# Performance work log

Hardware: AMD Instinct MI355X
Metric: run time of the kernel (lower is better)

Reference implementation:

```python
import jax, jax.numpy as jnp
import numpy as np


def conv_block(x, w1, b1, w2, b2):
    # 1x1 convs == per-pixel channel matmuls. x: [b, C, H, W]
    h = jax.nn.relu(jnp.einsum('bchw,oc->bohw', x, w1) + b1[None, :, None, None])
    return jnp.einsum('bchw,oc->bohw', h, w2) + b2[None, :, None, None]


def setup_inputs() -> dict:
    key = jax.random.key(0)
    ks = jax.random.split(key, 9)
    C, Ck = 256, 256 // 8
    bs, H, W = 4, 64, 64
    s_in = 1.0 / np.sqrt(C)
    s_k = 1.0 / np.sqrt(Ck)
    F_input = jax.random.normal(ks[0], (bs, C, H, W), dtype=jnp.float32)
    return {
        'F_input': F_input,
        'w1a': jax.random.normal(ks[1], (Ck, C), dtype=jnp.float32) * s_in,
        'b1a': jax.random.normal(ks[2], (Ck,), dtype=jnp.float32) * s_in,
        'w1b': jax.random.normal(ks[3], (Ck, Ck), dtype=jnp.float32) * s_k,
        'b1b': jax.random.normal(ks[4], (Ck,), dtype=jnp.float32) * s_k,
        'w2a': jax.random.normal(ks[5], (Ck, C), dtype=jnp.float32) * s_in,
        'b2a': jax.random.normal(ks[6], (Ck,), dtype=jnp.float32) * s_in,
        'w2b': jax.random.normal(ks[7], (Ck, Ck), dtype=jnp.float32) * s_k,
        'b2b': jax.random.normal(ks[8], (Ck,), dtype=jnp.float32) * s_k,
    }


def reference(F_input, w1a, b1a, w1b, b1b, w2a, b2a, w2b, b2b):
    bs, C, H, W = F_input.shape
    N = H * W
    q = conv_block(F_input, w1a, b1a, w1b, b1b).reshape(bs, -1, N)  # [b, Ck, N]
    k = conv_block(F_input, w2a, b2a, w2b, b2b).reshape(bs, -1, N)  # [b, Ck, N]
    # mm_1[b, n, m] = sum_c q[b, c, n] * k[b, c, m]
    scores = jnp.einsum('bcn,bcm->bnm', q, k)  # [b, N, N]
    S = jax.nn.softmax(scores, axis=-1)
    Fr = F_input.reshape(bs, C, N)
    # bmm(F_reshape, S^T): out[b, c, n] = sum_m F[b, c, m] * S[b, n, m]
    mm2 = jnp.einsum('bcm,bnm->bcn', Fr, S).reshape(bs, C, H, W)
    return F_input + mm2
```

## Files before the change

### kernel.cpp

```cpp
#include <hip/hip_runtime.h>
#include <math.h>

typedef __attribute__((ext_vector_type(4))) float f32x4;
typedef __attribute__((ext_vector_type(8))) short bf16x8;
typedef __attribute__((ext_vector_type(2))) unsigned int uint2v;
typedef __attribute__((ext_vector_type(4))) unsigned int uint4v;

#define LOG2E 1.4426950408889634f
#define MT 32
#define NIT 128

static __device__ __forceinline__ unsigned short f2bf(float f) {
  union { float f; unsigned int i; } u; u.f = f;
  unsigned int r = u.i + 0x7fffu + ((u.i >> 16) & 1u);
  return (unsigned short)(r >> 16);
}

typedef __attribute__((address_space(3))) unsigned int lds_u32;
typedef __attribute__((address_space(1))) unsigned int g_u32;

static __device__ __forceinline__ void gload_lds16(const unsigned short* g,
                                                   const unsigned short* l) {
  __builtin_amdgcn_global_load_lds(
      (const g_u32*)(unsigned long long)g,
      (lds_u32*)(unsigned int)(unsigned long long)l, 16, 0, 0);
}

__global__ __launch_bounds__(256) void k_wprep(const float* __restrict__ w1a,
                                               const float* __restrict__ w2a,
                                               float* __restrict__ w1aT,
                                               float* __restrict__ w2aT) {
  int i = blockIdx.x * 256 + threadIdx.x;
  if (i < 32 * 256) {
    int o = i >> 8, c = i & 255;
    w1aT[c * 32 + o] = w1a[i];
    w2aT[c * 32 + o] = w2a[i];
  }
}

__global__ __launch_bounds__(256) void k_cvt(const float* __restrict__ F,
                                             unsigned short* __restrict__ Fbf) {
  size_t i = ((size_t)blockIdx.x * 256 + threadIdx.x) * 8;
  f32x4 a = *(const f32x4*)(F + i);
  f32x4 b = *(const f32x4*)(F + i + 4);
  unsigned int u0 = (unsigned int)f2bf(a[0]) | ((unsigned int)f2bf(a[1]) << 16);
  unsigned int u1 = (unsigned int)f2bf(a[2]) | ((unsigned int)f2bf(a[3]) << 16);
  unsigned int u2 = (unsigned int)f2bf(b[0]) | ((unsigned int)f2bf(b[1]) << 16);
  unsigned int u3 = (unsigned int)f2bf(b[2]) | ((unsigned int)f2bf(b[3]) << 16);
  uint4v v = {u0, u1, u2, u3};
  *(uint4v*)(Fbf + i) = v;
}

__global__ __launch_bounds__(128) void k_qk(
    const float* __restrict__ F,
    const float* __restrict__ w1aT, const float* __restrict__ b1a,
    const float* __restrict__ w1b,  const float* __restrict__ b1b,
    const float* __restrict__ w2aT, const float* __restrict__ b2a,
    const float* __restrict__ w2b,  const float* __restrict__ b2b,
    unsigned short* __restrict__ qT,
    unsigned short* __restrict__ kT) {
  const int p = blockIdx.x & 1;
  const int nflat = (blockIdx.x >> 1) * 128 + threadIdx.x;
  const int b = nflat >> 12, n = nflat & 4095;
  const float* wA = p ? w2aT : w1aT;
  const float* bA = p ? b2a : b1a;
  const float* wB = p ? w2b : w1b;
  const float* bB = p ? b2b : b1b;
  const float* Fp = F + ((size_t)b * 256) * 4096 + n;

  float h[32];
#pragma unroll
  for (int o = 0; o < 32; ++o) h[o] = 0.f;

  float fa[8], fb[8];
#pragma unroll
  for (int j = 0; j < 8; ++j) fa[j] = Fp[(size_t)j * 4096];

  for (int cc = 0; cc < 256; cc += 16) {
#pragma unroll
    for (int j = 0; j < 8; ++j) fb[j] = Fp[(size_t)(cc + 8 + j) * 4096];
#pragma unroll
    for (int j = 0; j < 8; ++j)
#pragma unroll
      for (int o = 0; o < 32; ++o) h[o] += wA[(cc + j) * 32 + o] * fa[j];
    if (cc + 16 < 256) {
#pragma unroll
      for (int j = 0; j < 8; ++j) fa[j] = Fp[(size_t)(cc + 16 + j) * 4096];
    }
#pragma unroll
    for (int j = 0; j < 8; ++j)
#pragma unroll
      for (int o = 0; o < 32; ++o) h[o] += wA[(cc + 8 + j) * 32 + o] * fb[j];
  }
#pragma unroll
  for (int o = 0; o < 32; ++o) h[o] = fmaxf(h[o] + bA[o], 0.f);

  unsigned int pack[16];
#pragma unroll
  for (int o2 = 0; o2 < 32; o2 += 2) {
    float s0 = bB[o2], s1 = bB[o2 + 1];
#pragma unroll
    for (int o = 0; o < 32; ++o) {
      s0 += wB[o2 * 32 + o] * h[o];
      s1 += wB[(o2 + 1) * 32 + o] * h[o];
    }
    if (p == 0) { s0 *= LOG2E; s1 *= LOG2E; }
    pack[o2 >> 1] = (unsigned int)f2bf(s0) | ((unsigned int)f2bf(s1) << 16);
  }
  unsigned short* dst = (p ? kT : qT) + (size_t)nflat * 32;
  uint4v* d4 = (uint4v*)dst;
#pragma unroll
  for (int i = 0; i < 4; ++i) {
    uint4v v = {pack[4 * i], pack[4 * i + 1], pack[4 * i + 2], pack[4 * i + 3]};
    d4[i] = v;
  }
}

__global__ __launch_bounds__(256, 1) void k_attn(
    const unsigned short* __restrict__ qT,
    const unsigned short* __restrict__ kT,
    const unsigned short* __restrict__ Fbf,
    const float* __restrict__ F,
    float* __restrict__ out) {
  __shared__ unsigned short Vt[3][256 * MT];
  __shared__ unsigned short Pb[2][64 * MT];
  __shared__ float scl[2][64];
  __shared__ float linv[64];

  const int tid = threadIdx.x;
  const int w = tid >> 6;
  const int lane = tid & 63;
  const int lo = lane & 15;
  const int hi = lane >> 4;

  const int bid = (int)blockIdx.x;
  const int swz = (bid & 7) * 32 + (bid >> 3);
  const int b = swz >> 6;
  const int n0 = (swz & 63) << 6;

  const bf16x8 qfrag = *(const bf16x8*)(
      qT + ((size_t)(b << 12) + n0 + (w << 4) + lo) * 32 + (hi << 3));
  const unsigned short* kTb = kT + ((size_t)(b << 12)) * 32;
  const unsigned short* Fb = Fbf + ((size_t)b << 20);

  const int crow = lane >> 2;
  const int pch = lane & 3;

  f32x4 acc[4][4];
#pragma unroll
  for (int i = 0; i < 4; ++i)
#pragma unroll
    for (int j = 0; j < 4; ++j) acc[i][j] = (f32x4){0.f, 0.f, 0.f, 0.f};
  float mrun = -INFINITY, lrun = 0.f;

#pragma unroll
  for (int i = 0; i < 4; ++i) {
    int c = i * 64 + (w << 4) + crow;
    gload_lds16(Fb + (size_t)c * 4096 + ((pch ^ (c & 3)) << 3),
                &Vt[0][(i * 64 + (w << 4)) * MT]);
  }
  bf16x8 kc0 = *(const bf16x8*)(kTb + ((size_t)lo) * 32 + (hi << 3));
  bf16x8 kc1 = *(const bf16x8*)(kTb + ((size_t)(16 + lo)) * 32 + (hi << 3));

  int vb = 0, vn = 1;
  for (int t = 0; t < NIT; ++t) {
    if (t + 1 < NIT) {
#pragma unroll
      for (int i = 0; i < 4; ++i) {
        int c = i * 64 + (w << 4) + crow;
        gload_lds16(Fb + (size_t)c * 4096 + (size_t)(t + 1) * MT + ((pch ^ (c & 3)) << 3),
                    &Vt[vn][(i * 64 + (w << 4)) * MT]);
      }
    }
    bf16x8 kn0, kn1;
    if (t + 1 < NIT) {
      kn0 = *(const bf16x8*)(kTb + ((size_t)((t + 1) * MT) + lo) * 32 + (hi << 3));
      kn1 = *(const bf16x8*)(kTb + ((size_t)((t + 1) * MT) + 16 + lo) * 32 + (hi << 3));
    }
    f32x4 z = (f32x4){0.f, 0.f, 0.f, 0.f};
    f32x4 s0 = __builtin_amdgcn_mfma_f32_16x16x32_bf16(kc0, qfrag, z, 0, 0, 0);
    f32x4 s1 = __builtin_amdgcn_mfma_f32_16x16x32_bf16(kc1, qfrag, z, 0, 0, 0);

    float tmax = fmaxf(fmaxf(fmaxf(s0[0], s0[1]), fmaxf(s0[2], s0[3])),
                       fmaxf(fmaxf(s1[0], s1[1]), fmaxf(s1[2], s1[3])));
    tmax = fmaxf(tmax, __shfl_xor(tmax, 16));
    tmax = fmaxf(tmax, __shfl_xor(tmax, 32));
    float mnew = fmaxf(mrun, tmax);
    float sc = exp2f(mrun - mnew);
    mrun = mnew;
    float p00 = exp2f(s0[0] - mnew), p01 = exp2f(s0[1] - mnew);
    float p02 = exp2f(s0[2] - mnew), p03 = exp2f(s0[3] - mnew);
    float p10 = exp2f(s1[0] - mnew), p11 = exp2f(s1[1] - mnew);
    float p12 = exp2f(s1[2] - mnew), p13 = exp2f(s1[3] - mnew);
    float rsum = p00 + p01 + p02 + p03 + p10 + p11 + p12 + p13;
    rsum += __shfl_xor(rsum, 16);
    rsum += __shfl_xor(rsum, 32);
    lrun = lrun * sc + rsum;
    if (hi == 0) scl[t & 1][(w << 4) + lo] = sc;

    {
      const int qr = (w << 4) + lo;
      unsigned short* base = &Pb[t & 1][qr * MT];
      int ch0 = (hi >> 1), ch1 = 2 + (hi >> 1);
      uint2v v0 = {(unsigned int)f2bf(p00) | ((unsigned int)f2bf(p01) << 16),
                   (unsigned int)f2bf(p02) | ((unsigned int)f2bf(p03) << 16)};
      uint2v v1 = {(unsigned int)f2bf(p10) | ((unsigned int)f2bf(p11) << 16),
                   (unsigned int)f2bf(p12) | ((unsigned int)f2bf(p13) << 16)};
      *(uint2v*)(base + (((ch0 ^ (qr & 3)) << 3) | ((hi & 1) << 2))) = v0;
      *(uint2v*)(base + (((ch1 ^ (qr & 3)) << 3) | ((hi & 1) << 2))) = v1;
    }

    __syncthreads();

    {
      f32x4 sv[4];
      bool one = true;
#pragma unroll
      for (int qf = 0; qf < 4; ++qf) {
        sv[qf] = *(const f32x4*)&scl[t & 1][(qf << 4) + (hi << 2)];
        one = one && (sv[qf][0] == 1.f) && (sv[qf][1] == 1.f) &&
              (sv[qf][2] == 1.f) && (sv[qf][3] == 1.f);
      }
      if (!__all(one)) {
#pragma unroll
        for (int qf = 0; qf < 4; ++qf)
#pragma unroll
          for (int cs = 0; cs < 4; ++cs) acc[qf][cs] *= sv[qf];
      }
    }

    bf16x8 pf[4], vf[4];
#pragma unroll
    for (int qf = 0; qf < 4; ++qf) {
      int qr = (qf << 4) + lo;
      pf[qf] = *(const bf16x8*)&Pb[t & 1][qr * MT + ((hi ^ (qr & 3)) << 3)];
    }
#pragma unroll
    for (int cs = 0; cs < 4; ++cs) {
      int c = (w << 6) + (cs << 4) + lo;
      vf[cs] = *(const bf16x8*)&Vt[vb][c * MT + ((hi ^ (c & 3)) << 3)];
    }
#pragma unroll
    for (int qf = 0; qf < 4; ++qf)
#pragma unroll
      for (int cs = 0; cs < 4; ++cs)
        acc[qf][cs] = __builtin_amdgcn_mfma_f32_16x16x32_bf16(pf[qf], vf[cs], acc[qf][cs], 0, 0, 0);

    kc0 = kn0; kc1 = kn1;
    vb = vn; vn = (vn == 2) ? 0 : vn + 1;
  }

  if (hi == 0) linv[(w << 4) + lo] = 1.f / lrun;
  __syncthreads();
  f32x4 lv[4];
#pragma unroll
  for (int qf = 0; qf < 4; ++qf) lv[qf] = *(const f32x4*)&linv[(qf << 4) + (hi << 2)];
#pragma unroll
  for (int qf = 0; qf < 4; ++qf)
#pragma unroll
    for (int cs = 0; cs < 4; ++cs) {
      size_t idx = ((size_t)(b * 256 + (w << 6) + (cs << 4) + lo)) * 4096 +
                   n0 + (qf << 4) + (hi << 2);
      f32x4 fv = *(const f32x4*)(F + idx);
      *(f32x4*)(out + idx) = fv + acc[qf][cs] * lv[qf];
    }
}

extern "C" void kernel_launch(void* const* d_in, const int* in_sizes, int n_in,
                              void* d_out, int out_size, void* d_ws, size_t ws_size,
                              hipStream_t stream) {
  const float* F   = (const float*)d_in[0];
  const float* w1a = (const float*)d_in[1];
  const float* b1a = (const float*)d_in[2];
  const float* w1b = (const float*)d_in[3];
  const float* b1b = (const float*)d_in[4];
  const float* w2a = (const float*)d_in[5];
  const float* b2a = (const float*)d_in[6];
  const float* w2b = (const float*)d_in[7];
  const float* b2b = (const float*)d_in[8];
  float* out = (float*)d_out;

  char* ws = (char*)d_ws;
  float* w1aT = (float*)(ws);
  float* w2aT = (float*)(ws + 32768);
  unsigned short* Fbf = (unsigned short*)(ws + 65536);
  unsigned short* qT  = (unsigned short*)(ws + 65536 + 8388608);
  unsigned short* kT  = (unsigned short*)(ws + 65536 + 8388608 + 1048576);

  hipLaunchKernelGGL(k_wprep, dim3(32), dim3(256), 0, stream, w1a, w2a, w1aT, w2aT);
  hipLaunchKernelGGL(k_cvt, dim3(2048), dim3(256), 0, stream, F, Fbf);
  hipLaunchKernelGGL(k_qk, dim3(256), dim3(128), 0, stream,
                     F, w1aT, b1a, w1b, b1b, w2aT, b2a, w2b, b2b, qT, kT);
  hipLaunchKernelGGL(k_attn, dim3(256), dim3(256), 0, stream, qT, kT, Fbf, F, out);
}
```

Before: 342.7 us.

## Split attention across key partitions with combine kernel; fuse bf16 cast into qk

```diff
diff --git a/kernel.cpp b/kernel.cpp
--- a/kernel.cpp
+++ b/kernel.cpp
@@ -8,7 +8,6 @@
 
 #define LOG2E 1.4426950408889634f
 #define MT 32
-#define NIT 128
 
 static __device__ __forceinline__ unsigned short f2bf(float f) {
   union { float f; unsigned int i; } u; u.f = f;
@@ -38,113 +37,141 @@
   }
 }
 
-__global__ __launch_bounds__(256) void k_cvt(const float* __restrict__ F,
-                                             unsigned short* __restrict__ Fbf) {
-  size_t i = ((size_t)blockIdx.x * 256 + threadIdx.x) * 8;
-  f32x4 a = *(const f32x4*)(F + i);
-  f32x4 b = *(const f32x4*)(F + i + 4);
-  unsigned int u0 = (unsigned int)f2bf(a[0]) | ((unsigned int)f2bf(a[1]) << 16);
-  unsigned int u1 = (unsigned int)f2bf(a[2]) | ((unsigned int)f2bf(a[3]) << 16);
-  unsigned int u2 = (unsigned int)f2bf(b[0]) | ((unsigned int)f2bf(b[1]) << 16);
-  unsigned int u3 = (unsigned int)f2bf(b[2]) | ((unsigned int)f2bf(b[3]) << 16);
-  uint4v v = {u0, u1, u2, u3};
-  *(uint4v*)(Fbf + i) = v;
-}
-
-__global__ __launch_bounds__(128) void k_qk(
+__global__ __launch_bounds__(256) void k_qk(
     const float* __restrict__ F,
     const float* __restrict__ w1aT, const float* __restrict__ b1a,
     const float* __restrict__ w1b,  const float* __restrict__ b1b,
     const float* __restrict__ w2aT, const float* __restrict__ b2a,
     const float* __restrict__ w2b,  const float* __restrict__ b2b,
+    unsigned short* __restrict__ Fbf,
     unsigned short* __restrict__ qT,
     unsigned short* __restrict__ kT) {
-  const int p = blockIdx.x & 1;
-  const int nflat = (blockIdx.x >> 1) * 128 + threadIdx.x;
-  const int b = nflat >> 12, n = nflat & 4095;
-  const float* wA = p ? w2aT : w1aT;
-  const float* bA = p ? b2a : b1a;
-  const float* wB = p ? w2b : w1b;
-  const float* bB = p ? b2b : b1b;
-  const float* Fp = F + ((size_t)b * 256) * 4096 + n;
-
-  float h[32];
-#pragma unroll
-  for (int o = 0; o < 32; ++o) h[o] = 0.f;
+  __shared__ float hp[4][64][33];
+  const int tid = threadIdx.x;
+  const int nl = tid & 63;
+  const int cs = __builtin_amdgcn_readfirstlane(tid >> 6);
+  const int strip = blockIdx.x;
+  const int b = strip >> 6;
+  const int n0 = (strip & 63) << 6;
+  const int n = n0 + nl;
+
+  const float* Fp = F + ((size_t)(b * 256 + cs * 64)) * 4096 + n;
+  unsigned short* Fbp = Fbf + ((size_t)(b * 256 + cs * 64)) * 4096 + n;
+
+  float hq[32], hk[32];
+#pragma unroll
+  for (int o = 0; o < 32; ++o) { hq[o] = 0.f; hk[o] = 0.f; }
 
   float fa[8], fb[8];
 #pragma unroll
   for (int j = 0; j < 8; ++j) fa[j] = Fp[(size_t)j * 4096];
 
-  for (int cc = 0; cc < 256; cc += 16) {
-#pragma unroll
-    for (int j = 0; j < 8; ++j) fb[j] = Fp[(size_t)(cc + 8 + j) * 4096];
-#pragma unroll
-    for (int j = 0; j < 8; ++j)
-#pragma unroll
-      for (int o = 0; o < 32; ++o) h[o] += wA[(cc + j) * 32 + o] * fa[j];
-    if (cc + 16 < 256) {
-#pragma unroll
-      for (int j = 0; j < 8; ++j) fa[j] = Fp[(size_t)(cc + 16 + j) * 4096];
-    }
-#pragma unroll
-    for (int j = 0; j < 8; ++j)
-#pragma unroll
-      for (int o = 0; o < 32; ++o) h[o] += wA[(cc + 8 + j) * 32 + o] * fb[j];
-  }
-#pragma unroll
-  for (int o = 0; o < 32; ++o) h[o] = fmaxf(h[o] + bA[o], 0.f);
-
-  unsigned int pack[16];
-#pragma unroll
-  for (int o2 = 0; o2 < 32; o2 += 2) {
-    float s0 = bB[o2], s1 = bB[o2 + 1];
-#pragma unroll
-    for (int o = 0; o < 32; ++o) {
-      s0 += wB[o2 * 32 + o] * h[o];
-      s1 += wB[(o2 + 1) * 32 + o] * h[o];
-    }
-    if (p == 0) { s0 *= LOG2E; s1 *= LOG2E; }
-    pack[o2 >> 1] = (unsigned int)f2bf(s0) | ((unsigned int)f2bf(s1) << 16);
-  }
-  unsigned short* dst = (p ? kT : qT) + (size_t)nflat * 32;
-  uint4v* d4 = (uint4v*)dst;
-#pragma unroll
-  for (int i = 0; i < 4; ++i) {
-    uint4v v = {pack[4 * i], pack[4 * i + 1], pack[4 * i + 2], pack[4 * i + 3]};
-    d4[i] = v;
-  }
-}
-
-__global__ __launch_bounds__(256, 1) void k_attn(
+  for (int jj = 0; jj < 64; jj += 16) {
+#pragma unroll
+    for (int j = 0; j < 8; ++j) fb[j] = Fp[(size_t)(jj + 8 + j) * 4096];
+#pragma unroll
+    for (int j = 0; j < 8; ++j) {
+      Fbp[(size_t)(jj + j) * 4096] = f2bf(fa[j]);
+      const float* wq = w1aT + (cs * 64 + jj + j) * 32;
+      const float* wk = w2aT + (cs * 64 + jj + j) * 32;
+#pragma unroll
+      for (int o = 0; o < 32; ++o) { hq[o] += wq[o] * fa[j]; hk[o] += wk[o] * fa[j]; }
+    }
+    if (jj + 16 < 64) {
+#pragma unroll
+      for (int j = 0; j < 8; ++j) fa[j] = Fp[(size_t)(jj + 16 + j) * 4096];
+    }
+#pragma unroll
+    for (int j = 0; j < 8; ++j) {
+      Fbp[(size_t)(jj + 8 + j) * 4096] = f2bf(fb[j]);
+      const float* wq = w1aT + (cs * 64 + jj + 8 + j) * 32;
+      const float* wk = w2aT + (cs * 64 + jj + 8 + j) * 32;
+#pragma unroll
+      for (int o = 0; o < 32; ++o) { hq[o] += wq[o] * fb[j]; hk[o] += wk[o] * fb[j]; }
+    }
+  }
+
+#pragma unroll
+  for (int o = 0; o < 32; ++o) hp[cs][nl][o] = hq[o];
+  __syncthreads();
+  {
+    float h[32];
+#pragma unroll
+    for (int o = 0; o < 32; ++o)
+      h[o] = fmaxf(hp[0][nl][o] + hp[1][nl][o] + hp[2][nl][o] + hp[3][nl][o] + b1a[o], 0.f);
+    unsigned int pk[4];
+#pragma unroll
+    for (int oo = 0; oo < 8; oo += 2) {
+      float s0 = b1b[cs * 8 + oo], s1 = b1b[cs * 8 + oo + 1];
+#pragma unroll
+      for (int i = 0; i < 32; ++i) {
+        s0 += w1b[(cs * 8 + oo) * 32 + i] * h[i];
+        s1 += w1b[(cs * 8 + oo + 1) * 32 + i] * h[i];
+      }
+      s0 *= LOG2E; s1 *= LOG2E;
+      pk[oo >> 1] = (unsigned int)f2bf(s0) | ((unsigned int)f2bf(s1) << 16);
+    }
+    uint4v v = {pk[0], pk[1], pk[2], pk[3]};
+    *(uint4v*)(qT + ((size_t)(b * 4096 + n)) * 32 + cs * 8) = v;
+  }
+  __syncthreads();
+#pragma unroll
+  for (int o = 0; o < 32; ++o) hp[cs][nl][o] = hk[o];
+  __syncthreads();
+  {
+    float h[32];
+#pragma unroll
+    for (int o = 0; o < 32; ++o)
+      h[o] = fmaxf(hp[0][nl][o] + hp[1][nl][o] + hp[2][nl][o] + hp[3][nl][o] + b2a[o], 0.f);
+    unsigned int pk[4];
+#pragma unroll
+    for (int oo = 0; oo < 8; oo += 2) {
+      float s0 = b2b[cs * 8 + oo], s1 = b2b[cs * 8 + oo + 1];
+#pragma unroll
+      for (int i = 0; i < 32; ++i) {
+        s0 += w2b[(cs * 8 + oo) * 32 + i] * h[i];
+        s1 += w2b[(cs * 8 + oo + 1) * 32 + i] * h[i];
+      }
+      pk[oo >> 1] = (unsigned int)f2bf(s0) | ((unsigned int)f2bf(s1) << 16);
+    }
+    uint4v v = {pk[0], pk[1], pk[2], pk[3]};
+    *(uint4v*)(kT + ((size_t)(b * 4096 + n)) * 32 + cs * 8) = v;
+  }
+}
+
+__global__ __launch_bounds__(256, 4) void k_attn(
     const unsigned short* __restrict__ qT,
     const unsigned short* __restrict__ kT,
     const unsigned short* __restrict__ Fbf,
     const float* __restrict__ F,
-    float* __restrict__ out) {
-  __shared__ unsigned short Vt[3][256 * MT];
-  __shared__ unsigned short Pb[2][64 * MT];
-  __shared__ float scl[2][64];
-  __shared__ float linv[64];
+    float* __restrict__ out,
+    float* __restrict__ Opart,
+    float* __restrict__ Mpart,
+    float* __restrict__ Lpart,
+    int spl, int mtiles, int direct) {
+  __shared__ unsigned short Vt[256 * MT];
+  __shared__ unsigned short Pb[64 * MT];
+  __shared__ float scl[64];
 
   const int tid = threadIdx.x;
-  const int w = tid >> 6;
-  const int lane = tid & 63;
-  const int lo = lane & 15;
-  const int hi = lane >> 4;
+  const int w = tid >> 6, lane = tid & 63, lo = lane & 15, hi = lane >> 4;
 
   const int bid = (int)blockIdx.x;
-  const int swz = (bid & 7) * 32 + (bid >> 3);
-  const int b = swz >> 6;
-  const int n0 = (swz & 63) << 6;
+  int g, ns;
+  if (spl == 4)      { g = ((bid & 7) << 1) | (bid >> 9); ns = (bid >> 3) & 63; }
+  else if (spl == 2) { g = bid & 7;                       ns = bid >> 3; }
+  else               { int sz = (bid & 7) * 32 + (bid >> 3); g = sz >> 6; ns = sz & 63; }
+  const int b = (spl == 4) ? (g >> 2) : ((spl == 2) ? (g >> 1) : g);
+  const int s = (spl == 4) ? (g & 3) : ((spl == 2) ? (g & 1) : 0);
+  const int n0 = ns << 6;
+  const int mt0 = s * mtiles;
 
   const bf16x8 qfrag = *(const bf16x8*)(
       qT + ((size_t)(b << 12) + n0 + (w << 4) + lo) * 32 + (hi << 3));
   const unsigned short* kTb = kT + ((size_t)(b << 12)) * 32;
   const unsigned short* Fb = Fbf + ((size_t)b << 20);
 
-  const int crow = lane >> 2;
-  const int pch = lane & 3;
+  const int crow = lane >> 2, pch = lane & 3;
 
   f32x4 acc[4][4];
 #pragma unroll
@@ -156,27 +183,13 @@
 #pragma unroll
   for (int i = 0; i < 4; ++i) {
     int c = i * 64 + (w << 4) + crow;
-    gload_lds16(Fb + (size_t)c * 4096 + ((pch ^ (c & 3)) << 3),
-                &Vt[0][(i * 64 + (w << 4)) * MT]);
-  }
-  bf16x8 kc0 = *(const bf16x8*)(kTb + ((size_t)lo) * 32 + (hi << 3));
-  bf16x8 kc1 = *(const bf16x8*)(kTb + ((size_t)(16 + lo)) * 32 + (hi << 3));
-
-  int vb = 0, vn = 1;
-  for (int t = 0; t < NIT; ++t) {
-    if (t + 1 < NIT) {
-#pragma unroll
-      for (int i = 0; i < 4; ++i) {
-        int c = i * 64 + (w << 4) + crow;
-        gload_lds16(Fb + (size_t)c * 4096 + (size_t)(t + 1) * MT + ((pch ^ (c & 3)) << 3),
-                    &Vt[vn][(i * 64 + (w << 4)) * MT]);
-      }
-    }
-    bf16x8 kn0, kn1;
-    if (t + 1 < NIT) {
-      kn0 = *(const bf16x8*)(kTb + ((size_t)((t + 1) * MT) + lo) * 32 + (hi << 3));
-      kn1 = *(const bf16x8*)(kTb + ((size_t)((t + 1) * MT) + 16 + lo) * 32 + (hi << 3));
-    }
+    gload_lds16(Fb + (size_t)c * 4096 + (mt0 << 5) + ((pch ^ (c & 3)) << 3),
+                &Vt[(i * 64 + (w << 4)) * MT]);
+  }
+  bf16x8 kc0 = *(const bf16x8*)(kTb + ((size_t)((mt0 << 5) + lo)) * 32 + (hi << 3));
+  bf16x8 kc1 = *(const bf16x8*)(kTb + ((size_t)((mt0 << 5) + 16 + lo)) * 32 + (hi << 3));
+
+  for (int t = 0; t < mtiles; ++t) {
     f32x4 z = (f32x4){0.f, 0.f, 0.f, 0.f};
     f32x4 s0 = __builtin_amdgcn_mfma_f32_16x16x32_bf16(kc0, qfrag, z, 0, 0, 0);
     f32x4 s1 = __builtin_amdgcn_mfma_f32_16x16x32_bf16(kc1, qfrag, z, 0, 0, 0);
@@ -196,11 +209,10 @@
     rsum += __shfl_xor(rsum, 16);
     rsum += __shfl_xor(rsum, 32);
     lrun = lrun * sc + rsum;
-    if (hi == 0) scl[t & 1][(w << 4) + lo] = sc;
-
+    if (hi == 0) scl[(w << 4) + lo] = sc;
     {
       const int qr = (w << 4) + lo;
-      unsigned short* base = &Pb[t & 1][qr * MT];
+      unsigned short* base = &Pb[qr * MT];
       int ch0 = (hi >> 1), ch1 = 2 + (hi >> 1);
       uint2v v0 = {(unsigned int)f2bf(p00) | ((unsigned int)f2bf(p01) << 16),
                    (unsigned int)f2bf(p02) | ((unsigned int)f2bf(p03) << 16)};
@@ -217,7 +229,7 @@
       bool one = true;
 #pragma unroll
       for (int qf = 0; qf < 4; ++qf) {
-        sv[qf] = *(const f32x4*)&scl[t & 1][(qf << 4) + (hi << 2)];
+        sv[qf] = *(const f32x4*)&scl[(qf << 4) + (hi << 2)];
         one = one && (sv[qf][0] == 1.f) && (sv[qf][1] == 1.f) &&
               (sv[qf][2] == 1.f) && (sv[qf][3] == 1.f);
       }
@@ -225,45 +237,121 @@
 #pragma unroll
         for (int qf = 0; qf < 4; ++qf)
 #pragma unroll
-          for (int cs = 0; cs < 4; ++cs) acc[qf][cs] *= sv[qf];
-      }
-    }
-
+          for (int cs2 = 0; cs2 < 4; ++cs2) acc[qf][cs2] *= sv[qf];
+      }
+    }
     bf16x8 pf[4], vf[4];
 #pragma unroll
     for (int qf = 0; qf < 4; ++qf) {
       int qr = (qf << 4) + lo;
-      pf[qf] = *(const bf16x8*)&Pb[t & 1][qr * MT + ((hi ^ (qr & 3)) << 3)];
-    }
-#pragma unroll
-    for (int cs = 0; cs < 4; ++cs) {
-      int c = (w << 6) + (cs << 4) + lo;
-      vf[cs] = *(const bf16x8*)&Vt[vb][c * MT + ((hi ^ (c & 3)) << 3)];
-    }
+      pf[qf] = *(const bf16x8*)&Pb[qr * MT + ((hi ^ (qr & 3)) << 3)];
+    }
+#pragma unroll
+    for (int cs2 = 0; cs2 < 4; ++cs2) {
+      int c = (w << 6) + (cs2 << 4) + lo;
+      vf[cs2] = *(const bf16x8*)&Vt[c * MT + ((hi ^ (c & 3)) << 3)];
+    }
+    __builtin_amdgcn_s_setprio(1);
 #pragma unroll
     for (int qf = 0; qf < 4; ++qf)
 #pragma unroll
-      for (int cs = 0; cs < 4; ++cs)
-        acc[qf][cs] = __builtin_amdgcn_mfma_f32_16x16x32_bf16(pf[qf], vf[cs], acc[qf][cs], 0, 0, 0);
-
-    kc0 = kn0; kc1 = kn1;
-    vb = vn; vn = (vn == 2) ? 0 : vn + 1;
-  }
-
-  if (hi == 0) linv[(w << 4) + lo] = 1.f / lrun;
+      for (int cs2 = 0; cs2 < 4; ++cs2)
+        acc[qf][cs2] = __builtin_amdgcn_mfma_f32_16x16x32_bf16(pf[qf], vf[cs2], acc[qf][cs2], 0, 0, 0);
+    __builtin_amdgcn_s_setprio(0);
+
+    __syncthreads();
+
+    if (t + 1 < mtiles) {
+      int mo = (mt0 + t + 1) << 5;
+#pragma unroll
+      for (int i = 0; i < 4; ++i) {
+        int c = i * 64 + (w << 4) + crow;
+        gload_lds16(Fb + (size_t)c * 4096 + mo + ((pch ^ (c & 3)) << 3),
+                    &Vt[(i * 64 + (w << 4)) * MT]);
+      }
+      kc0 = *(const bf16x8*)(kTb + ((size_t)(mo + lo)) * 32 + (hi << 3));
+      kc1 = *(const bf16x8*)(kTb + ((size_t)(mo + 16 + lo)) * 32 + (hi << 3));
+    }
+  }
+
+  if (direct) {
+    if (hi == 0) scl[(w << 4) + lo] = 1.f / lrun;
+    __syncthreads();
+    f32x4 lv[4];
+#pragma unroll
+    for (int qf = 0; qf < 4; ++qf) lv[qf] = *(const f32x4*)&scl[(qf << 4) + (hi << 2)];
+#pragma unroll
+    for (int qf = 0; qf < 4; ++qf)
+#pragma unroll
+      for (int cs2 = 0; cs2 < 4; ++cs2) {
+        size_t idx = ((size_t)(b * 256 + (w << 6) + (cs2 << 4) + lo)) * 4096 +
+                     n0 + (qf << 4) + (hi << 2);
+        f32x4 fv = *(const f32x4*)(F + idx);
+        *(f32x4*)(out + idx) = fv + acc[qf][cs2] * lv[qf];
+      }
+  } else {
+    const int bp = (b * spl + s) * 64 + ns;
+    if (hi == 0) {
+      Mpart[bp * 64 + (w << 4) + lo] = mrun;
+      Lpart[bp * 64 + (w << 4) + lo] = lrun;
+    }
+    float* Ob = Opart + (size_t)bp * 256 * 64;
+#pragma unroll
+    for (int qf = 0; qf < 4; ++qf)
+#pragma unroll
+      for (int cs2 = 0; cs2 < 4; ++cs2) {
+        int c = (w << 6) + (cs2 << 4) + lo;
+        *(f32x4*)(Ob + (size_t)c * 64 + (qf << 4) + (hi << 2)) = acc[qf][cs2];
+      }
+  }
+}
+
+__global__ __launch_bounds__(256, 4) void k_comb(
+    const float* __restrict__ F, const float* __restrict__ Opart,
+    const float* __restrict__ Mpart, const float* __restrict__ Lpart,
+    float* __restrict__ out, int spl) {
+  __shared__ float a[4][64];
+  const int cid = (int)blockIdx.x;
+  const int b = cid >> 8, ns = (cid >> 2) & 63, cq = cid & 3;
+  const int tid = threadIdx.x, q = tid & 63, ci = tid >> 6;
+  const int n0 = ns << 6;
+
+  if (tid < 64) {
+    float mv[4], lv[4];
+    float M = -INFINITY;
+#pragma unroll
+    for (int s2 = 0; s2 < 4; ++s2)
+      if (s2 < spl) {
+        int bp = (b * spl + s2) * 64 + ns;
+        mv[s2] = Mpart[bp * 64 + q];
+        lv[s2] = Lpart[bp * 64 + q];
+        M = fmaxf(M, mv[s2]);
+      }
+    float L = 0.f;
+#pragma unroll
+    for (int s2 = 0; s2 < 4; ++s2)
+      if (s2 < spl) { mv[s2] = exp2f(mv[s2] - M); L += mv[s2] * lv[s2]; }
+    float Li = 1.f / L;
+#pragma unroll
+    for (int s2 = 0; s2 < 4; ++s2)
+      if (s2 < spl) a[s2][q] = mv[s2] * Li;
+  }
   __syncthreads();
-  f32x4 lv[4];
-#pragma unroll
-  for (int qf = 0; qf < 4; ++qf) lv[qf] = *(const f32x4*)&linv[(qf << 4) + (hi << 2)];
-#pragma unroll
-  for (int qf = 0; qf < 4; ++qf)
-#pragma unroll
-    for (int cs = 0; cs < 4; ++cs) {
-      size_t idx = ((size_t)(b * 256 + (w << 6) + (cs << 4) + lo)) * 4096 +
-                   n0 + (qf << 4) + (hi << 2);
-      f32x4 fv = *(const f32x4*)(F + idx);
-      *(f32x4*)(out + idx) = fv + acc[qf][cs] * lv[qf];
-    }
+  float aq[4];
+#pragma unroll
+  for (int s2 = 0; s2 < 4; ++s2) aq[s2] = (s2 < spl) ? a[s2][q] : 0.f;
+
+#pragma unroll 4
+  for (int cc = 0; cc < 16; ++cc) {
+    int c = (cq << 6) + (ci << 4) + cc;
+    float accv = 0.f;
+#pragma unroll
+    for (int s2 = 0; s2 < 4; ++s2)
+      if (s2 < spl)
+        accv += aq[s2] * Opart[((size_t)((b * spl + s2) * 64 + ns) * 256 + c) * 64 + q];
+    size_t idx = ((size_t)(b * 256 + c)) * 4096 + n0 + q;
+    out[idx] = F[idx] + accv;
+  }
 }
 
 extern "C" void kernel_launch(void* const* d_in, const int* in_sizes, int n_in,
@@ -283,13 +371,26 @@
   char* ws = (char*)d_ws;
   float* w1aT = (float*)(ws);
   float* w2aT = (float*)(ws + 32768);
-  unsigned short* Fbf = (unsigned short*)(ws + 65536);
-  unsigned short* qT  = (unsigned short*)(ws + 65536 + 8388608);
-  unsigned short* kT  = (unsigned short*)(ws + 65536 + 8388608 + 1048576);
+  unsigned short* qT  = (unsigned short*)(ws + 65536);
+  unsigned short* kT  = (unsigned short*)(ws + 65536 + 1048576);
+  unsigned short* Fbf = (unsigned short*)(ws + 65536 + 2097152);
+  const size_t obase = 65536 + 2097152 + 8388608;
+
+  int spl = 1, direct = 1;
+  const size_t oSz1 = 16777216, mlSz1 = 65536;
+  if (ws_size >= obase + 4 * (oSz1 + 2 * mlSz1)) { spl = 4; direct = 0; }
+  else if (ws_size >= obase + 2 * (oSz1 + 2 * mlSz1)) { spl = 2; direct = 0; }
+
+  float* Opart = (float*)(ws + obase);
+  float* Mpart = (float*)(ws + obase + (size_t)spl * oSz1);
+  float* Lpart = (float*)(ws + obase + (size_t)spl * oSz1 + (size_t)spl * mlSz1);
 
   hipLaunchKernelGGL(k_wprep, dim3(32), dim3(256), 0, stream, w1a, w2a, w1aT, w2aT);
-  hipLaunchKernelGGL(k_cvt, dim3(2048), dim3(256), 0, stream, F, Fbf);
-  hipLaunchKernelGGL(k_qk, dim3(256), dim3(128), 0, stream,
-                     F, w1aT, b1a, w1b, b1b, w2aT, b2a, w2b, b2b, qT, kT);
-  hipLaunchKernelGGL(k_attn, dim3(256), dim3(256), 0, stream, qT, kT, Fbf, F, out);
-}
+  hipLaunchKernelGGL(k_qk, dim3(256), dim3(256), 0, stream,
+                     F, w1aT, b1a, w1b, b1b, w2aT, b2a, w2b, b2b, Fbf, qT, kT);
+  hipLaunchKernelGGL(k_attn, dim3(256 * spl), dim3(256), 0, stream,
+                     qT, kT, Fbf, F, out, Opart, Mpart, Lpart, spl, 128 / spl, direct);
+  if (!direct)
+    hipLaunchKernelGGL(k_comb, dim3(1024), dim3(256), 0, stream,
+                       F, Opart, Mpart, Lpart, out, spl);
+}
```

Result: faster. 289.2 us (-15.6%).
